# Kernel tuning notes

Hardware: AMD Instinct MI355X
Metric: run time of the kernel (lower is better)

The kernel has to match this reference:

```python
import jax, jax.numpy as jnp
import numpy as np

N_NODES = 100000
N_EDGES = 800000
D = 128
N_HEADS = 8
D_HEAD = D // N_HEADS


def setup_inputs() -> dict:
    key = jax.random.key(0)
    ks = jax.random.split(key, 8)
    x = jax.random.normal(ks[0], (N_NODES, D), dtype=jnp.float32)
    src = jax.random.randint(ks[1], (N_EDGES,), 0, N_NODES, dtype=jnp.int32)
    dst = jax.random.randint(ks[2], (N_EDGES,), 0, N_NODES, dtype=jnp.int32)
    s = 1.0 / np.sqrt(D)
    # torch nn.Linear convention: y = x @ W.T + b, W ~ U(-1/sqrt(fan_in), ...)
    W_qkv = jax.random.uniform(ks[3], (3 * D, D), jnp.float32, -s, s)
    b_qkv = jax.random.uniform(ks[4], (3 * D,), jnp.float32, -s, s)
    W_out = jax.random.uniform(ks[5], (D, D), jnp.float32, -s, s)
    b_out = jax.random.uniform(ks[6], (D,), jnp.float32, -s, s)
    return {"x": x, "W_qkv": W_qkv, "b_qkv": b_qkv, "W_out": W_out,
            "b_out": b_out, "src": src, "dst": dst}


def reference(x, W_qkv, b_qkv, W_out, b_out, src, dst):
    N = x.shape[0]
    coef = D_HEAD ** -0.5
    qkv = (x @ W_qkv.T + b_qkv).reshape(N, N_HEADS, 3 * D_HEAD)
    q = qkv[..., :D_HEAD]          # [N, H, dh]
    k = qkv[..., D_HEAD:2 * D_HEAD]
    v = qkv[..., 2 * D_HEAD:]
    # u_dot_v: per-edge dot of source k and destination q -> [E, H]
    scores = jnp.einsum('ehd,ehd->eh', k[src], q[dst]) * coef
    # edge_softmax: softmax over edges grouped by destination node
    m = jax.ops.segment_max(scores, dst, num_segments=N)
    m = jnp.where(jnp.isfinite(m), m, 0.0)  # guard zero in-degree nodes
    p = jnp.exp(scores - m[dst])
    denom = jax.ops.segment_sum(p, dst, num_segments=N)
    probs = p / denom[dst]                   # [E, H]
    # u_mul_e_sum: weighted aggregation of source v into destination
    out = jax.ops.segment_sum(v[src] * probs[:, :, None], dst, num_segments=N)
    out = out.reshape(N, D)
    return out @ W_out.T + b_out
```

## Files before the change

### kernel.cpp

```cpp
#include <hip/hip_runtime.h>
#include <hip/hip_bf16.h>

#define N_NODES 100000
#define N_EDGES 800000
#define NB1 98

typedef __attribute__((ext_vector_type(8))) short short8;
typedef __attribute__((ext_vector_type(4))) float f32x4;
typedef __attribute__((ext_vector_type(2))) unsigned int u32x2;

__device__ __forceinline__ float bf2f(ushort u) {
    union { unsigned i; float f; } x; x.i = ((unsigned)u) << 16; return x.f;
}
__device__ __forceinline__ ushort f2bf(float f) {
    union { float f; unsigned u; } x { f };
    unsigned r = x.u + 0x7FFF + ((x.u >> 16) & 1);
    return (ushort)(r >> 16);
}

__global__ __launch_bounds__(128) void prep_and_count(
    const float* __restrict__ Wq, const float* __restrict__ bq,
    const float* __restrict__ Wo, const int* __restrict__ dst,
    ushort* __restrict__ Wqb, float* __restrict__ bqp, ushort* __restrict__ Wob,
    int* __restrict__ counts)
{
    int j = blockIdx.x;
    if (j < 384) {
        int h = j / 48, r = j % 48, p;
        if (r < 16)      p = h * 16 + r;
        else if (r < 32) { int d = r - 16; p = 128 + (h * 8 + (d >> 1)) * 4 + (d & 1); }
        else             { int d = r - 32; p = 128 + (h * 8 + (d >> 1)) * 4 + 2 + (d & 1); }
        Wqb[(size_t)p * 128 + threadIdx.x] = f2bf(Wq[(size_t)j * 128 + threadIdx.x]);
        if (threadIdx.x == 0) bqp[p] = bq[j];
    } else if (j < 512) {
        int j2 = j - 384;
        Wob[(size_t)j2 * 128 + threadIdx.x] = f2bf(Wo[(size_t)j2 * 128 + threadIdx.x]);
    } else {
        int e = (j - 512) * 128 + threadIdx.x;
        if (e < N_EDGES) atomicAdd(&counts[dst[e]], 1);
    }
}

template<int A_F32, int OUT_BF16>
__global__ __launch_bounds__(256) void gemm_mfma(
    const void* __restrict__ Av, const ushort* __restrict__ B,
    const float* __restrict__ bias, void* __restrict__ Cv,
    int M, int ldc)
{
    __shared__ ushort As[128][72];
    __shared__ ushort Bs[128][72];
    const int t = threadIdx.x;
    const int lane = t & 63;
    const int w = t >> 6;
    const int wm = w >> 1, wn = w & 1;
    const int n0 = blockIdx.y * 128;
    const int j0 = blockIdx.x * 128;

    f32x4 acc[4][4];
    #pragma unroll
    for (int i = 0; i < 4; ++i)
        #pragma unroll
        for (int j = 0; j < 4; ++j) acc[i][j] = (f32x4){0.f, 0.f, 0.f, 0.f};

    for (int kb = 0; kb < 128; kb += 64) {
        #pragma unroll
        for (int it = 0; it < 4; ++it) {
            int c = it * 256 + t;
            int row = c >> 3, g = c & 7;
            int ar = n0 + row; if (ar >= M) ar = M - 1;
            if (A_F32) {
                const float* ap = (const float*)Av + (size_t)ar * 128 + kb + g * 8;
                float4 a0 = *reinterpret_cast<const float4*>(ap);
                float4 a1 = *reinterpret_cast<const float4*>(ap + 4);
                short8 o;
                o[0] = (short)f2bf(a0.x); o[1] = (short)f2bf(a0.y);
                o[2] = (short)f2bf(a0.z); o[3] = (short)f2bf(a0.w);
                o[4] = (short)f2bf(a1.x); o[5] = (short)f2bf(a1.y);
                o[6] = (short)f2bf(a1.z); o[7] = (short)f2bf(a1.w);
                *reinterpret_cast<short8*>(&As[row][g * 8]) = o;
            } else {
                *reinterpret_cast<short8*>(&As[row][g * 8]) =
                    *reinterpret_cast<const short8*>(
                        (const ushort*)Av + (size_t)ar * 128 + kb + g * 8);
            }
            *reinterpret_cast<short8*>(&Bs[row][g * 8]) =
                *reinterpret_cast<const short8*>(B + (size_t)(j0 + row) * 128 + kb + g * 8);
        }
        __syncthreads();
        #pragma unroll
        for (int kf = 0; kf < 2; ++kf) {
            short8 af[4], bfr[4];
            #pragma unroll
            for (int mf = 0; mf < 4; ++mf)
                af[mf] = *reinterpret_cast<const short8*>(
                    &As[wm * 64 + mf * 16 + (lane & 15)][kf * 32 + (lane >> 4) * 8]);
            #pragma unroll
            for (int nf = 0; nf < 4; ++nf)
                bfr[nf] = *reinterpret_cast<const short8*>(
                    &Bs[wn * 64 + nf * 16 + (lane & 15)][kf * 32 + (lane >> 4) * 8]);
            #pragma unroll
            for (int mf = 0; mf < 4; ++mf)
                #pragma unroll
                for (int nf = 0; nf < 4; ++nf)
                    acc[mf][nf] = __builtin_amdgcn_mfma_f32_16x16x32_bf16(
                        bfr[nf], af[mf], acc[mf][nf], 0, 0, 0);
        }
        __syncthreads();
    }

    const int r = lane & 15, c4 = (lane >> 4) * 4;
    #pragma unroll
    for (int mf = 0; mf < 4; ++mf) {
        int row = n0 + wm * 64 + mf * 16 + r;
        if (row >= M) continue;
        #pragma unroll
        for (int nf = 0; nf < 4; ++nf) {
            int col = j0 + wn * 64 + nf * 16 + c4;
            f32x4 a = acc[mf][nf];
            float v0 = a[0] + bias[col],     v1 = a[1] + bias[col + 1];
            float v2 = a[2] + bias[col + 2], v3 = a[3] + bias[col + 3];
            if (OUT_BF16) {
                u32x2 u;
                u[0] = (unsigned)f2bf(v0) | ((unsigned)f2bf(v1) << 16);
                u[1] = (unsigned)f2bf(v2) | ((unsigned)f2bf(v3) << 16);
                *reinterpret_cast<u32x2*>((ushort*)Cv + (size_t)row * ldc + col) = u;
            } else {
                float4 o = {v0, v1, v2, v3};
                *reinterpret_cast<float4*>((float*)Cv + (size_t)row * ldc + col) = o;
            }
        }
    }
}

__global__ __launch_bounds__(1024) void scan1(
    const int* __restrict__ counts, int* __restrict__ row_start,
    int* __restrict__ bsums)
{
    __shared__ int sd[1024];
    int t = threadIdx.x, i = blockIdx.x * 1024 + t;
    int v = (i < N_NODES) ? counts[i] : 0;
    sd[t] = v; __syncthreads();
    for (int off = 1; off < 1024; off <<= 1) {
        int x = (t >= off) ? sd[t - off] : 0;
        __syncthreads();
        sd[t] += x;
        __syncthreads();
    }
    if (i < N_NODES) row_start[i] = sd[t] - v;
    if (t == 1023) bsums[blockIdx.x] = sd[1023];
}

__global__ __launch_bounds__(128) void scan2(
    const int* __restrict__ bsums, int* __restrict__ boffs)
{
    __shared__ int sd[128];
    int t = threadIdx.x;
    int v = (t < NB1) ? bsums[t] : 0;
    sd[t] = v; __syncthreads();
    for (int off = 1; off < 128; off <<= 1) {
        int x = (t >= off) ? sd[t - off] : 0;
        __syncthreads();
        sd[t] += x;
        __syncthreads();
    }
    if (t < NB1) boffs[t] = sd[t] - v;
}

__global__ __launch_bounds__(256) void scan3(
    int* __restrict__ row_start, const int* __restrict__ boffs)
{
    int i = blockIdx.x * 256 + threadIdx.x;
    if (i < N_NODES) row_start[i] += boffs[i >> 10];
    if (i == 0) row_start[N_NODES] = N_EDGES;
}

__global__ __launch_bounds__(256) void fill_csr(
    const int* __restrict__ src, const int* __restrict__ dst,
    const int* __restrict__ row_start, int* __restrict__ fillc,
    int* __restrict__ csr_src)
{
    int e = blockIdx.x * 256 + threadIdx.x;
    if (e >= N_EDGES) return;
    int d = dst[e];
    int pos = row_start[d] + atomicAdd(&fillc[d], 1);
    csr_src[pos] = src[e];
}

__global__ __launch_bounds__(256) void fused_attn(
    const ushort* __restrict__ qkvp, const int* __restrict__ row_start,
    const int* __restrict__ csr_src, ushort* __restrict__ attnb)
{
    int node = (blockIdx.x * 256 + threadIdx.x) >> 6;
    if (node >= N_NODES) return;
    int lane = threadIdx.x & 63;

    unsigned qb = *reinterpret_cast<const unsigned*>(
        qkvp + (size_t)node * 384 + lane * 2);
    float q0 = bf2f((ushort)qb), q1 = bf2f((ushort)(qb >> 16));

    int beg = row_start[node], end = row_start[node + 1];
    float denom = 0.f, a0 = 0.f, a1 = 0.f;
    const ushort* kvbase = qkvp + 128 + lane * 4;

#define GATHER(s, u) u = *reinterpret_cast<const u32x2*>(kvbase + (size_t)(s) * 384);
#define EDGE(u) { \
        float ps = bf2f((ushort)u[0]) * q0 + bf2f((ushort)(u[0] >> 16)) * q1; \
        ps += __shfl_xor(ps, 1); \
        ps += __shfl_xor(ps, 2); \
        ps += __shfl_xor(ps, 4); \
        float p = __expf(ps * 0.25f); \
        denom += p; \
        a0 += p * bf2f((ushort)u[1]); \
        a1 += p * bf2f((ushort)(u[1] >> 16)); }

    int i = beg;
    for (; i + 8 <= end; i += 8) {
        int s0 = csr_src[i],     s1 = csr_src[i + 1];
        int s2 = csr_src[i + 2], s3 = csr_src[i + 3];
        int s4 = csr_src[i + 4], s5 = csr_src[i + 5];
        int s6 = csr_src[i + 6], s7 = csr_src[i + 7];
        u32x2 u0, u1, u2, u3, u4, u5, u6, u7;
        GATHER(s0, u0); GATHER(s1, u1); GATHER(s2, u2); GATHER(s3, u3);
        GATHER(s4, u4); GATHER(s5, u5); GATHER(s6, u6); GATHER(s7, u7);
        EDGE(u0); EDGE(u1); EDGE(u2); EDGE(u3);
        EDGE(u4); EDGE(u5); EDGE(u6); EDGE(u7);
    }
    for (; i < end; ++i) {
        int s = csr_src[i];
        u32x2 u;
        GATHER(s, u);
        EDGE(u);
    }
#undef GATHER
#undef EDGE

    float inv = (end > beg) ? 1.f / denom : 0.f;
    unsigned o = ((unsigned)f2bf(a1 * inv) << 16) | (unsigned)f2bf(a0 * inv);
    *reinterpret_cast<unsigned*>(attnb + (size_t)node * 128 + lane * 2) = o;
}

extern "C" void kernel_launch(void* const* d_in, const int* in_sizes, int n_in,
                              void* d_out, int out_size, void* d_ws, size_t ws_size,
                              hipStream_t stream) {
    const float* x     = (const float*)d_in[0];
    const float* W_qkv = (const float*)d_in[1];
    const float* b_qkv = (const float*)d_in[2];
    const float* W_out = (const float*)d_in[3];
    const float* b_out = (const float*)d_in[4];
    const int*   src   = (const int*)d_in[5];
    const int*   dst   = (const int*)d_in[6];
    float* out = (float*)d_out;

    char* w = (char*)d_ws;
    ushort* qkvp     = (ushort*)(w);
    ushort* attnb    = (ushort*)(w + 76800000);
    ushort* Wqb      = (ushort*)(w + 102400000);
    ushort* Wob      = (ushort*)(w + 102498304);
    float*  bqp      = (float*)(w + 102531072);
    int*    counts   = (int*)(w + 102532608);
    int*    fillc    = (int*)(w + 102932608);
    int*    row_start= (int*)(w + 103332608);
    int*    bsums    = (int*)(w + 103732624);
    int*    boffs    = (int*)(w + 103733136);
    int*    csr_src  = (int*)(w + 103733648);

    hipMemsetAsync(counts, 0, 800000, stream);

    prep_and_count<<<6762, 128, 0, stream>>>(W_qkv, b_qkv, W_out, dst,
                                             Wqb, bqp, Wob, counts);

    gemm_mfma<1, 1><<<dim3(3, 782), 256, 0, stream>>>(
        (const void*)x, Wqb, bqp, (void*)qkvp, N_NODES, 384);

    scan1<<<NB1, 1024, 0, stream>>>(counts, row_start, bsums);
    scan2<<<1, 128, 0, stream>>>(bsums, boffs);
    scan3<<<391, 256, 0, stream>>>(row_start, boffs);
    fill_csr<<<3125, 256, 0, stream>>>(src, dst, row_start, fillc, csr_src);

    fused_attn<<<25000, 256, 0, stream>>>(qkvp, row_start, csr_src, attnb);

    gemm_mfma<0, 0><<<dim3(1, 782), 256, 0, stream>>>(
        (const void*)attnb, Wob, b_out, (void*)out, N_NODES, 128);
}
```

Measured before the change: 317.6 us.

## Pre-convert x to bf16, record atomic ranks, single-block scan, smaller gather unroll

x is now converted to bf16 once in the prep kernel, so the QKV GEMM no longer re-reads and re-converts fp32 x in each of its three column-tile blocks. The counting pass stores each edge's atomic rank, which lets fill_csr place edges without a second atomic pass and removes the fillc buffer and its memset. The three-kernel scan is replaced by one 1024-thread block that has each thread scan a chunk of 98 counts. The attention gather unroll drops from 8 to 4 edges, lowering register pressure at the cost of fewer loads in flight. The risks are an extra bf16 copy of x in memory, a serial single-block scan, and a large per-thread local array.

```diff
diff --git a/kernel.cpp b/kernel.cpp
--- a/kernel.cpp
+++ b/kernel.cpp
@@ -3,7 +3,6 @@
 
 #define N_NODES 100000
 #define N_EDGES 800000
-#define NB1 98
 
 typedef __attribute__((ext_vector_type(8))) short short8;
 typedef __attribute__((ext_vector_type(4))) float f32x4;
@@ -18,11 +17,12 @@
     return (ushort)(r >> 16);
 }
 
-__global__ __launch_bounds__(128) void prep_and_count(
+__global__ __launch_bounds__(128) void prep_all(
     const float* __restrict__ Wq, const float* __restrict__ bq,
-    const float* __restrict__ Wo, const int* __restrict__ dst,
+    const float* __restrict__ Wo, const float* __restrict__ x,
+    const int* __restrict__ dst,
     ushort* __restrict__ Wqb, float* __restrict__ bqp, ushort* __restrict__ Wob,
-    int* __restrict__ counts)
+    ushort* __restrict__ xb, int* __restrict__ counts, int* __restrict__ rank)
 {
     int j = blockIdx.x;
     if (j < 384) {
@@ -35,15 +35,21 @@
     } else if (j < 512) {
         int j2 = j - 384;
         Wob[(size_t)j2 * 128 + threadIdx.x] = f2bf(Wo[(size_t)j2 * 128 + threadIdx.x]);
+    } else if (j < 25512) {
+        int i = (j - 512) * 128 + threadIdx.x;
+        float4 v = reinterpret_cast<const float4*>(x)[i];
+        ushort4 o;
+        o.x = f2bf(v.x); o.y = f2bf(v.y); o.z = f2bf(v.z); o.w = f2bf(v.w);
+        reinterpret_cast<ushort4*>(xb)[i] = o;
     } else {
-        int e = (j - 512) * 128 + threadIdx.x;
-        if (e < N_EDGES) atomicAdd(&counts[dst[e]], 1);
-    }
-}
-
-template<int A_F32, int OUT_BF16>
+        int e = (j - 25512) * 128 + threadIdx.x;
+        if (e < N_EDGES) rank[e] = atomicAdd(&counts[dst[e]], 1);
+    }
+}
+
+template<int OUT_BF16>
 __global__ __launch_bounds__(256) void gemm_mfma(
-    const void* __restrict__ Av, const ushort* __restrict__ B,
+    const ushort* __restrict__ A, const ushort* __restrict__ B,
     const float* __restrict__ bias, void* __restrict__ Cv,
     int M, int ldc)
 {
@@ -68,21 +74,8 @@
             int c = it * 256 + t;
             int row = c >> 3, g = c & 7;
             int ar = n0 + row; if (ar >= M) ar = M - 1;
-            if (A_F32) {
-                const float* ap = (const float*)Av + (size_t)ar * 128 + kb + g * 8;
-                float4 a0 = *reinterpret_cast<const float4*>(ap);
-                float4 a1 = *reinterpret_cast<const float4*>(ap + 4);
-                short8 o;
-                o[0] = (short)f2bf(a0.x); o[1] = (short)f2bf(a0.y);
-                o[2] = (short)f2bf(a0.z); o[3] = (short)f2bf(a0.w);
-                o[4] = (short)f2bf(a1.x); o[5] = (short)f2bf(a1.y);
-                o[6] = (short)f2bf(a1.z); o[7] = (short)f2bf(a1.w);
-                *reinterpret_cast<short8*>(&As[row][g * 8]) = o;
-            } else {
-                *reinterpret_cast<short8*>(&As[row][g * 8]) =
-                    *reinterpret_cast<const short8*>(
-                        (const ushort*)Av + (size_t)ar * 128 + kb + g * 8);
-            }
+            *reinterpret_cast<short8*>(&As[row][g * 8]) =
+                *reinterpret_cast<const short8*>(A + (size_t)ar * 128 + kb + g * 8);
             *reinterpret_cast<short8*>(&Bs[row][g * 8]) =
                 *reinterpret_cast<const short8*>(B + (size_t)(j0 + row) * 128 + kb + g * 8);
         }
@@ -132,58 +125,47 @@
     }
 }
 
-__global__ __launch_bounds__(1024) void scan1(
-    const int* __restrict__ counts, int* __restrict__ row_start,
-    int* __restrict__ bsums)
+#define CHUNK 98
+__global__ __launch_bounds__(1024) void scan_one(
+    const int* __restrict__ counts, int* __restrict__ row_start)
 {
     __shared__ int sd[1024];
-    int t = threadIdx.x, i = blockIdx.x * 1024 + t;
-    int v = (i < N_NODES) ? counts[i] : 0;
-    sd[t] = v; __syncthreads();
+    const int t = threadIdx.x;
+    const int base = t * CHUNK;
+    int lc[CHUNK];
+    int sum = 0;
+    #pragma unroll 7
+    for (int i = 0; i < CHUNK; ++i) {
+        int idx = base + i;
+        int v = (idx < N_NODES) ? counts[idx] : 0;
+        lc[i] = v;
+        sum += v;
+    }
+    sd[t] = sum; __syncthreads();
     for (int off = 1; off < 1024; off <<= 1) {
         int x = (t >= off) ? sd[t - off] : 0;
         __syncthreads();
         sd[t] += x;
         __syncthreads();
     }
-    if (i < N_NODES) row_start[i] = sd[t] - v;
-    if (t == 1023) bsums[blockIdx.x] = sd[1023];
-}
-
-__global__ __launch_bounds__(128) void scan2(
-    const int* __restrict__ bsums, int* __restrict__ boffs)
-{
-    __shared__ int sd[128];
-    int t = threadIdx.x;
-    int v = (t < NB1) ? bsums[t] : 0;
-    sd[t] = v; __syncthreads();
-    for (int off = 1; off < 128; off <<= 1) {
-        int x = (t >= off) ? sd[t - off] : 0;
-        __syncthreads();
-        sd[t] += x;
-        __syncthreads();
-    }
-    if (t < NB1) boffs[t] = sd[t] - v;
-}
-
-__global__ __launch_bounds__(256) void scan3(
-    int* __restrict__ row_start, const int* __restrict__ boffs)
-{
-    int i = blockIdx.x * 256 + threadIdx.x;
-    if (i < N_NODES) row_start[i] += boffs[i >> 10];
-    if (i == 0) row_start[N_NODES] = N_EDGES;
+    int run = sd[t] - sum;
+    #pragma unroll 7
+    for (int i = 0; i < CHUNK; ++i) {
+        int idx = base + i;
+        if (idx < N_NODES) row_start[idx] = run;
+        run += lc[i];
+    }
+    if (t == 0) row_start[N_NODES] = N_EDGES;
 }
 
 __global__ __launch_bounds__(256) void fill_csr(
     const int* __restrict__ src, const int* __restrict__ dst,
-    const int* __restrict__ row_start, int* __restrict__ fillc,
+    const int* __restrict__ rank, const int* __restrict__ row_start,
     int* __restrict__ csr_src)
 {
     int e = blockIdx.x * 256 + threadIdx.x;
     if (e >= N_EDGES) return;
-    int d = dst[e];
-    int pos = row_start[d] + atomicAdd(&fillc[d], 1);
-    csr_src[pos] = src[e];
+    csr_src[row_start[dst[e]] + rank[e]] = src[e];
 }
 
 __global__ __launch_bounds__(256) void fused_attn(
@@ -214,16 +196,12 @@
         a1 += p * bf2f((ushort)(u[1] >> 16)); }
 
     int i = beg;
-    for (; i + 8 <= end; i += 8) {
+    for (; i + 4 <= end; i += 4) {
         int s0 = csr_src[i],     s1 = csr_src[i + 1];
         int s2 = csr_src[i + 2], s3 = csr_src[i + 3];
-        int s4 = csr_src[i + 4], s5 = csr_src[i + 5];
-        int s6 = csr_src[i + 6], s7 = csr_src[i + 7];
-        u32x2 u0, u1, u2, u3, u4, u5, u6, u7;
+        u32x2 u0, u1, u2, u3;
         GATHER(s0, u0); GATHER(s1, u1); GATHER(s2, u2); GATHER(s3, u3);
-        GATHER(s4, u4); GATHER(s5, u5); GATHER(s6, u6); GATHER(s7, u7);
         EDGE(u0); EDGE(u1); EDGE(u2); EDGE(u3);
-        EDGE(u4); EDGE(u5); EDGE(u6); EDGE(u7);
     }
     for (; i < end; ++i) {
         int s = csr_src[i];
@@ -254,31 +232,28 @@
     char* w = (char*)d_ws;
     ushort* qkvp     = (ushort*)(w);
     ushort* attnb    = (ushort*)(w + 76800000);
-    ushort* Wqb      = (ushort*)(w + 102400000);
-    ushort* Wob      = (ushort*)(w + 102498304);
-    float*  bqp      = (float*)(w + 102531072);
-    int*    counts   = (int*)(w + 102532608);
-    int*    fillc    = (int*)(w + 102932608);
-    int*    row_start= (int*)(w + 103332608);
-    int*    bsums    = (int*)(w + 103732624);
-    int*    boffs    = (int*)(w + 103733136);
-    int*    csr_src  = (int*)(w + 103733648);
-
-    hipMemsetAsync(counts, 0, 800000, stream);
-
-    prep_and_count<<<6762, 128, 0, stream>>>(W_qkv, b_qkv, W_out, dst,
-                                             Wqb, bqp, Wob, counts);
-
-    gemm_mfma<1, 1><<<dim3(3, 782), 256, 0, stream>>>(
-        (const void*)x, Wqb, bqp, (void*)qkvp, N_NODES, 384);
-
-    scan1<<<NB1, 1024, 0, stream>>>(counts, row_start, bsums);
-    scan2<<<1, 128, 0, stream>>>(bsums, boffs);
-    scan3<<<391, 256, 0, stream>>>(row_start, boffs);
-    fill_csr<<<3125, 256, 0, stream>>>(src, dst, row_start, fillc, csr_src);
+    ushort* xb       = (ushort*)(w + 102400000);
+    ushort* Wqb      = (ushort*)(w + 128000000);
+    ushort* Wob      = (ushort*)(w + 128098304);
+    float*  bqp      = (float*)(w + 128131072);
+    int*    counts   = (int*)(w + 128132608);
+    int*    row_start= (int*)(w + 128532608);
+    int*    rank     = (int*)(w + 128932624);
+    int*    csr_src  = (int*)(w + 132132624);
+
+    hipMemsetAsync(counts, 0, 400000, stream);
+
+    prep_all<<<31762, 128, 0, stream>>>(W_qkv, b_qkv, W_out, x, dst,
+                                        Wqb, bqp, Wob, xb, counts, rank);
+
+    gemm_mfma<1><<<dim3(3, 782), 256, 0, stream>>>(
+        xb, Wqb, bqp, (void*)qkvp, N_NODES, 384);
+
+    scan_one<<<1, 1024, 0, stream>>>(counts, row_start);
+    fill_csr<<<3125, 256, 0, stream>>>(src, dst, rank, row_start, csr_src);
 
     fused_attn<<<25000, 256, 0, stream>>>(qkvp, row_start, csr_src, attnb);
 
-    gemm_mfma<0, 0><<<dim3(1, 782), 256, 0, stream>>>(
-        (const void*)attnb, Wob, b_out, (void*)out, N_NODES, 128);
-}
+    gemm_mfma<0><<<dim3(1, 782), 256, 0, stream>>>(
+        attnb, Wob, b_out, (void*)out, N_NODES, 128);
+}
```

Result: slower. 549.5 us (+73.0%).
